# Performance work log

Measured on AMD Instinct MI355X. Metric: run time of the kernel, lower is better.

The kernel has to match this reference:

```python
import jax, jax.numpy as jnp
import numpy as np

NUM_LEVELS = 8
SQRT2 = float(np.sqrt(2.0))
LOG2 = float(np.log(2.0))


def _e8_roots():
    # 240 E8 roots: 112 of form (+-1,+-1,0^6) and 128 of form (+-1/2)^8 with even # of minus signs
    roots = []
    for i in range(8):
        for j in range(i + 1, 8):
            for si in (1.0, -1.0):
                for sj in (1.0, -1.0):
                    v = np.zeros(8, dtype=np.float32)
                    v[i] = si
                    v[j] = sj
                    roots.append(v)
    for bits in range(256):
        signs = np.array([1.0 if (bits >> k) & 1 == 0 else -1.0 for k in range(8)], dtype=np.float32)
        if int((signs < 0).sum()) % 2 == 0:
            roots.append(0.5 * signs)
    return np.stack(roots)  # [240, 8]


def setup_inputs() -> dict:
    key = jax.random.key(0)
    ks = jax.random.split(key, 12)
    B = 262144
    return {
        "observation": jax.random.normal(ks[0], (B, 14), jnp.float32),
        "proj_w1": jax.random.normal(ks[1], (32, 14), jnp.float32) * (1.0 / np.sqrt(14)),
        "proj_b1": jnp.zeros((32,), jnp.float32),
        "proj_w2": jax.random.normal(ks[2], (8, 32), jnp.float32) * (1.0 / np.sqrt(32)),
        "proj_b2": jnp.zeros((8,), jnp.float32),
        "level_embeddings": jax.random.normal(ks[3], (NUM_LEVELS, 240, 52), jnp.float32) * 0.02,
        "base_control_params": jax.random.normal(ks[4], (240, 4), jnp.float32) * 0.1,
        "residual_control_params": jax.random.normal(ks[5], (NUM_LEVELS - 1, 240, 4), jnp.float32) * 0.02,
        "base_complexity": jnp.zeros((240,), jnp.float32),  # log(initial_complexity=1.0)
        "log_decay": jnp.array([0.5 * np.log(240.0)], jnp.float32),  # log(sqrt(240))
        "refine_w1": jax.random.normal(ks[6], (52, 52), jnp.float32) * (1.0 / np.sqrt(52)),
        "refine_b1": jnp.zeros((52,), jnp.float32),
        "refine_w2": jax.random.normal(ks[7], (52, 52), jnp.float32) * (1.0 / np.sqrt(52)),
        "refine_b2": jnp.zeros((52,), jnp.float32),
        "refine_gate": jnp.array([0.1], jnp.float32),
    }


def reference(observation, proj_w1, proj_b1, proj_w2, proj_b2, level_embeddings,
              base_control_params, residual_control_params, base_complexity,
              log_decay, refine_w1, refine_b1, refine_w2, refine_b2, refine_gate):
    roots = jnp.asarray(_e8_roots())                                  # [240, 8]
    roots_norm = roots / jnp.linalg.norm(roots, axis=-1, keepdims=True)

    # G2 -> E8 projection: Linear(14->32) -> GELU -> Linear(32->8), L2-normalize * sqrt(2)
    h = jax.nn.gelu(observation @ proj_w1.T + proj_b1, approximate=False)
    q = h @ proj_w2.T + proj_b2                                       # [B, 8]
    q = q / jnp.maximum(jnp.linalg.norm(q, axis=-1, keepdims=True), 1e-12) * SQRT2

    decay = jnp.exp(log_decay[0])
    r2 = jnp.sum(roots * roots, axis=-1)                              # [240]

    # Residual E8 quantization: sequential cdist + argmin + gather chain
    residual = q
    indices = []
    for level in range(NUM_LEVELS):
        scale = 2.0 / decay ** level
        scaled = residual / scale                                     # [B, 8]
        x2 = jnp.sum(scaled * scaled, axis=-1, keepdims=True)         # [B, 1]
        d2 = jnp.maximum(x2 + r2[None, :] - 2.0 * scaled @ roots.T, 0.0)  # [B, 240]
        idx = jnp.argmin(d2, axis=-1)                                 # [B]
        indices.append(idx)
        residual = residual - roots[idx] * scale

    # Base level: soft attention over 240 roots with MDL prior
    sims = q @ roots_norm.T                                           # [B, 240]
    logits = sims - base_complexity[None, :] * LOG2
    attn = jax.nn.softmax(logits, axis=-1)                            # temperature = 1.0
    embedding = attn @ level_embeddings[0]                            # [B, 52]
    control = attn @ base_control_params                              # [B, 4]

    # Residual levels: hard-index gathers with 1/decay^level scaling
    for level in range(1, NUM_LEVELS):
        inv_ld = 1.0 / decay ** level
        idx = indices[level]
        embedding = embedding + level_embeddings[level][idx] * inv_ld
        control = control + residual_control_params[level - 1][idx] * inv_ld

    # Gated refinement MLP
    refined = jax.nn.gelu(embedding @ refine_w1.T + refine_b1, approximate=False) @ refine_w2.T + refine_b2
    embedding = embedding + jax.nn.sigmoid(refine_gate[0]) * refined

    return jnp.concatenate([embedding, control], axis=-1)             # [B, 56]
```

## Files before the change

### kernel.cpp

```cpp
#include <hip/hip_runtime.h>
#include <hip/hip_bf16.h>
#include <math.h>

#define TPB  256
#define RTPB 128
#define EPS_GAP 1e-4f
#define LTAB 13440
#define LDSZ 13680

typedef unsigned int u32;
typedef unsigned long long u64;
typedef __attribute__((ext_vector_type(8))) short bf16x8;
typedef __attribute__((ext_vector_type(4))) float f32x4;

__device__ __forceinline__ int scan_fast(const float* x, float scale,
                                         float* residual, bool protect, bool& flag){
    float aa[8]; int neg=0; float S=0.f;
    #pragma unroll
    for (int k=0;k<8;k++){
        float v=x[k]; float av=fabsf(v);
        aa[k]=av; S+=av; neg |= (v<0.f)?(1<<k):0;
    }
    float t1=-1e30f,t2=-1e30f,t3=-1e30f; int p1=0,p2=0;
    #pragma unroll
    for (int k=0;k<8;k++){
        float v=aa[k];
        bool g1=v>t1, g2=v>t2, g3=v>t3;
        t3 = g2 ? t2 : (g3 ? v : t3);
        t2 = g1 ? t1 : (g2 ? v : t2);
        p2 = g1 ? p1 : (g2 ? k : p2);
        t1 = g1 ? v : t1;
        p1 = g1 ? k : p1;
    }
    float n1=1e30f,n2v=1e30f; int m1=0;
    #pragma unroll
    for (int k=0;k<8;k++){
        float v=aa[k];
        bool l1=v<n1, l2=v<n2v;
        n2v = l1 ? n1 : (l2 ? v : n2v);
        n1  = l1 ? v : n1;
        m1  = l1 ? k : m1;
    }
    int bi = min(p1,p2), bj = max(p1,p2);
    float pv = 2.f*(t1+t2), pr = 2.f*(t1+t3);
    int par = __builtin_popcount((unsigned)neg)&1;
    float hv, hr; int hb;
    if (par==0){ hv=S;          hb=neg;           hr=S-2.f*(n1+n2v); }
    else       { hv=S-2.f*n1;   hb=neg^(1<<m1);   hr=S-2.f*n2v; }
    bool pair = (pv >= hv);
    float best = pair? pv: hv, alt = pair? hv: pv;
    float second = fmaxf(alt, fmaxf(pr,hr));
    if (protect) flag = flag || ((best-second) < EPS_GAP);
    int s = (((neg>>bi)&1)<<1) | ((neg>>bj)&1);
    int pidx = 4*(7*bi - ((bi*(bi-1))>>1) + (bj-bi-1)) + s;
    int hidx = 112 + (hb>>1);
    float sI = ((neg>>bi)&1)? scale : -scale;
    float sJ = ((neg>>bj)&1)? scale : -scale;
    #pragma unroll
    for (int k=0;k<8;k++){
        float cp = ((k==bi)? sI:0.f) + ((k==bj)? sJ:0.f);
        float ch = ((hb>>k)&1)? 0.5f*scale : -0.5f*scale;
        residual[k] += (pair? cp : ch);
    }
    return pair? pidx : hidx;
}

__device__ __forceinline__ int scan_fast_f64(const double* x, double scale,
                                             double* residual){
    double aa[8]; int neg=0; double S=0.0;
    #pragma unroll
    for (int k=0;k<8;k++){
        double v=x[k]; double av=fabs(v);
        aa[k]=av; S+=av; neg |= (v<0.0)?(1<<k):0;
    }
    double t1=-1e300,t2=-1e300; int p1=0,p2=0;
    #pragma unroll
    for (int k=0;k<8;k++){
        double v=aa[k];
        bool g1=v>t1, g2=v>t2;
        t2 = g1 ? t1 : (g2 ? v : t2);
        p2 = g1 ? p1 : (g2 ? k : p2);
        t1 = g1 ? v : t1;
        p1 = g1 ? k : p1;
    }
    double n1=1e300; int m1=0;
    #pragma unroll
    for (int k=0;k<8;k++){
        double v=aa[k];
        bool l1=v<n1;
        n1 = l1 ? v : n1;
        m1 = l1 ? k : m1;
    }
    int bi = min(p1,p2), bj = max(p1,p2);
    double pv = 2.0*(t1+t2);
    int par = __builtin_popcount((unsigned)neg)&1;
    double hv; int hb;
    if (par==0){ hv=S;          hb=neg; }
    else       { hv=S-2.0*n1;   hb=neg^(1<<m1); }
    bool pair = (pv >= hv);
    int s = (((neg>>bi)&1)<<1) | ((neg>>bj)&1);
    int pidx = 4*(7*bi - ((bi*(bi-1))>>1) + (bj-bi-1)) + s;
    int hidx = 112 + (hb>>1);
    double sI = ((neg>>bi)&1)? scale : -scale;
    double sJ = ((neg>>bj)&1)? scale : -scale;
    #pragma unroll
    for (int k=0;k<8;k++){
        double cp = ((k==bi)? sI:0.0) + ((k==bj)? sJ:0.0);
        double ch = ((hb>>k)&1)? 0.5*scale : -0.5*scale;
        residual[k] += (pair? cp : ch);
    }
    return pair? pidx : hidx;
}

__device__ __forceinline__ void phaseB(const float* __restrict__ L, float* T,
    const float* qf,
    int i1,int i2,int i3,int i4,int i5,int i6,int i7, float decay,
    const float* __restrict__ lemb, const float* __restrict__ rcpar,
    float* __restrict__ orow)
{
    const float IS2 = 0.70710678118654752f;
    const float HS2 = 0.35355339059327376f;
    const float LG2 = 0.69314718055994531f;
    float hi16[16];
    {
        float a01p=qf[0]+qf[1], a01m=qf[0]-qf[1];
        float a23p=qf[2]+qf[3], a23m=qf[2]-qf[3];
        float a45p=qf[4]+qf[5], a45m=qf[4]-qf[5];
        float a67p=qf[6]+qf[7], a67m=qf[6]-qf[7];
        float s01[4]={a01p,-a01m,a01m,-a01p};
        float s23[4]={a23p,-a23m,a23m,-a23p};
        float s45[4]={a45p,-a45m,a45m,-a45p};
        float s67[4]={a67p,-a67m,a67m,-a67p};
        #pragma unroll
        for (int p=0;p<16;p++){ T[8+p]=s01[p&3]+s23[(p>>2)&3]; hi16[p]=s45[p&3]+s67[(p>>2)&3]; }
        #pragma unroll
        for (int k=0;k<8;k++) T[k]=qf[k];
    }
    float emb[56], den=0.f;
    #pragma unroll
    for (int k=0;k<56;k++) emb[k]=0.f;

    auto proc = [&](float sims, int j){
        float e = __expf(sims - L[LTAB + j]*LG2);
        den += e;
        const float4* Lr = (const float4*)(L + j*56);
        #pragma unroll
        for (int t=0;t<14;t++){
            float4 v = Lr[t];
            emb[4*t+0]=fmaf(e,v.x,emb[4*t+0]); emb[4*t+1]=fmaf(e,v.y,emb[4*t+1]);
            emb[4*t+2]=fmaf(e,v.z,emb[4*t+2]); emb[4*t+3]=fmaf(e,v.w,emb[4*t+3]);
        }
    };
    #pragma unroll
    for (int h=0;h<16;h++){
        float hv = hi16[h];
        int ph = __builtin_popcount(h)&1;
        #pragma unroll 1
        for (int m=0;m<8;m++){
            int lo = (m<<1) | ((__builtin_popcount(m)&1)^ph);
            proc((T[8+lo]+hv)*HS2, 112 + (h<<3) + m);
        }
    }
    {
        int ii=0, jn=1;
        #pragma unroll 1
        for (int pc=0;pc<28;++pc){
            float a=T[ii], b=T[jn];
            float p=a+b, mm=a-b;
            proc( p*IS2, 4*pc+0);
            proc( mm*IS2,4*pc+1);
            proc(-mm*IS2,4*pc+2);
            proc(-p*IS2, 4*pc+3);
            if (++jn==8){ ++ii; jn=ii+1; }
        }
    }
    float rden = 1.f/den;
    #pragma unroll
    for (int k=0;k<56;k++) emb[k] *= rden;

    {
        float dp = decay;
        #define DO_G(LVL, IV) { \
            float ild = 1.0f/dp; \
            const float4* ep4 = (const float4*)(lemb + ((size_t)(LVL)*240 + (size_t)(IV))*52); \
            _Pragma("unroll") for (int t4=0;t4<13;t4++){ float4 v=ep4[t4]; \
                emb[4*t4+0]=fmaf(ild,v.x,emb[4*t4+0]); emb[4*t4+1]=fmaf(ild,v.y,emb[4*t4+1]); \
                emb[4*t4+2]=fmaf(ild,v.z,emb[4*t4+2]); emb[4*t4+3]=fmaf(ild,v.w,emb[4*t4+3]); } \
            float4 cv = *(const float4*)(rcpar + ((size_t)((LVL)-1)*240 + (size_t)(IV))*4); \
            emb[52]=fmaf(ild,cv.x,emb[52]); emb[53]=fmaf(ild,cv.y,emb[53]); \
            emb[54]=fmaf(ild,cv.z,emb[54]); emb[55]=fmaf(ild,cv.w,emb[55]); \
            dp *= decay; }
        DO_G(1,i1) DO_G(2,i2) DO_G(3,i3) DO_G(4,i4) DO_G(5,i5) DO_G(6,i6) DO_G(7,i7)
        #undef DO_G
    }
    float4* o4 = (float4*)orow;
    #pragma unroll
    for (int t=0;t<14;t++)
        o4[t] = make_float4(emb[4*t], emb[4*t+1], emb[4*t+2], emb[4*t+3]);
}

__device__ __forceinline__ void stageL(float* L, int tid, int tpb,
    const float* __restrict__ lemb, const float* __restrict__ bcp,
    const float* __restrict__ bcx)
{
    for (int t = tid; t < LTAB; t += tpb){
        int j = t/56, c = t - j*56;
        L[t] = (c < 52) ? lemb[j*52 + c] : bcp[j*4 + (c-52)];
    }
    for (int t = tid; t < 240; t += tpb) L[LTAB + t] = bcx[t];
}

__device__ __forceinline__ unsigned short f2bf(float x){
    union{float f; u32 u;} c; c.f = x;
    u32 u = c.u + 0x7fffu + ((c.u>>16)&1u);
    return (unsigned short)(u>>16);
}
__device__ __forceinline__ u32 pk2(float a, float b){
    union { __hip_bfloat162 h; u32 u; } cv;
    cv.h = __float22bfloat162_rn(make_float2(a,b));
    return cv.u;
}

#define BT_PITCH 264
#define E_PITCH  260
#define SCR_PITCH 68

#define EP4(i,jn,J,W) { \
    float P=(qf[i]+qf[jn])*IS2, M=(qf[i]-qf[jn])*IS2; \
    float e0=__expf(fmaf(-LG2,bcxL[(J)+0],P)); \
    float e1=__expf(fmaf(-LG2,bcxL[(J)+1],M)); \
    float e2=__expf(fmaf(-LG2,bcxL[(J)+2],-M)); \
    float e3=__expf(fmaf(-LG2,bcxL[(J)+3],-P)); \
    den += ((e0+e1)+(e2+e3)); \
    ESH[((W)+0)*E_PITCH + tid]=pk2(e0,e1); \
    ESH[((W)+1)*E_PITCH + tid]=pk2(e2,e3); }

#define LOV(Lx) (s01[(Lx)&3]+s23[(Lx)>>2])
#define EH8(h,J,W,L0,L1,L2,L3,L4,L5,L6,L7) { \
    float hv=s45[(h)&3]+s67[(h)>>2]; \
    float e0=__expf(fmaf(-LG2,bcxL[(J)+0],(LOV(L0)+hv)*HS2)); \
    float e1=__expf(fmaf(-LG2,bcxL[(J)+1],(LOV(L1)+hv)*HS2)); \
    float e2=__expf(fmaf(-LG2,bcxL[(J)+2],(LOV(L2)+hv)*HS2)); \
    float e3=__expf(fmaf(-LG2,bcxL[(J)+3],(LOV(L3)+hv)*HS2)); \
    float e4=__expf(fmaf(-LG2,bcxL[(J)+4],(LOV(L4)+hv)*HS2)); \
    float e5=__expf(fmaf(-LG2,bcxL[(J)+5],(LOV(L5)+hv)*HS2)); \
    float e6=__expf(fmaf(-LG2,bcxL[(J)+6],(LOV(L6)+hv)*HS2)); \
    float e7=__expf(fmaf(-LG2,bcxL[(J)+7],(LOV(L7)+hv)*HS2)); \
    den += (((e0+e1)+(e2+e3))+((e4+e5)+(e6+e7))); \
    ESH[((W)+0)*E_PITCH + tid]=pk2(e0,e1); \
    ESH[((W)+1)*E_PITCH + tid]=pk2(e2,e3); \
    ESH[((W)+2)*E_PITCH + tid]=pk2(e4,e5); \
    ESH[((W)+3)*E_PITCH + tid]=pk2(e6,e7); }

#define EFLUSH(c) { \
    union { u32 u[4]; bf16x8 v; } Af; \
    const unsigned short* bp = BtT + pp*BT_PITCH + qq*8 + (c)*32; \
    bf16x8 b0 = *(const bf16x8*)(const void*)(bp); \
    bf16x8 b1 = *(const bf16x8*)(const void*)(bp + 16*BT_PITCH); \
    bf16x8 b2 = *(const bf16x8*)(const void*)(bp + 32*BT_PITCH); \
    bf16x8 b3 = *(const bf16x8*)(const void*)(bp + 48*BT_PITCH); \
    _Pragma("unroll") for (int s4=0;s4<4;s4++){ \
        const u32* ep = ESH + (4*qq)*E_PITCH + wbase + 16*s4 + pp; \
        Af.u[0]=ep[0]; Af.u[1]=ep[E_PITCH]; Af.u[2]=ep[2*E_PITCH]; Af.u[3]=ep[3*E_PITCH]; \
        acc[s4][0]=__builtin_amdgcn_mfma_f32_16x16x32_bf16(Af.v,b0,acc[s4][0],0,0,0); \
        acc[s4][1]=__builtin_amdgcn_mfma_f32_16x16x32_bf16(Af.v,b1,acc[s4][1],0,0,0); \
        acc[s4][2]=__builtin_amdgcn_mfma_f32_16x16x32_bf16(Af.v,b2,acc[s4][2],0,0,0); \
        acc[s4][3]=__builtin_amdgcn_mfma_f32_16x16x32_bf16(Af.v,b3,acc[s4][3],0,0,0); \
    } }

__global__ __launch_bounds__(TPB) void e8_phaseA(
    const float* __restrict__ g_obs,
    const float* __restrict__ pw1, const float* __restrict__ pb1,
    const float* __restrict__ pw2, const float* __restrict__ pb2,
    const float* __restrict__ glogdecay,
    u32* __restrict__ cnt, u32* __restrict__ list,
    unsigned char* __restrict__ flags, int useCompact,
    float* __restrict__ out, int B)
{
    __shared__ float obsF[TPB*17];
    const int tid = threadIdx.x;
    const int row = blockIdx.x*TPB + tid;
    const bool active = row < B;
    const int lane = tid & 63;

    {
        const size_t base = (size_t)blockIdx.x*TPB*14;
        const size_t lim  = (size_t)B*14;
        for (int t = tid; t < TPB*14; t += TPB){
            size_t g = base + (size_t)t;
            float v = (g < lim) ? g_obs[g] : 0.f;
            int r = t/14, c = t - r*14;
            obsF[r*17 + c] = v;
        }
    }
    __syncthreads();

    float qf[8];
    int idxs[8] = {0,0,0,0,0,0,0,0};
    bool flag = false;
    {
        float ob[14];
        #pragma unroll
        for (int j=0;j<14;j++) ob[j]=obsF[tid*17+j];
        float qa[8];
        #pragma unroll
        for (int m=0;m<8;m++) qa[m]=pb2[m];
        #pragma unroll 1
        for (int k=0;k<32;k++){
            float a = pb1[k];
            #pragma unroll
            for (int j=0;j<14;j++) a = fmaf(pw1[k*14+j], ob[j], a);
            float h = 0.5f*a*(1.f+erff(a*0.70710678f));
            #pragma unroll
            for (int m=0;m<8;m++) qa[m] = fmaf(pw2[m*32+k], h, qa[m]);
        }
        float n2=0.f;
        #pragma unroll
        for (int m=0;m<8;m++) n2 = fmaf(qa[m],qa[m],n2);
        float nr = fmaxf(sqrtf(n2), 1e-12f);
        float sc = 1.41421356237309505f/nr;
        float residual[8];
        #pragma unroll
        for (int m=0;m<8;m++){ qf[m]=qa[m]*sc; residual[m]=qf[m]; }

        float decay = expf(glogdecay[0]);
        float dpow = 1.f;
        #pragma unroll
        for (int lvl=0; lvl<8; ++lvl){
            float rs = 0.5f*dpow;
            float x[8];
            #pragma unroll
            for (int k=0;k<8;k++) x[k]=residual[k]*rs;
            idxs[lvl] = scan_fast(x, 2.f/dpow, residual, (lvl<3), flag);
            dpow *= decay;
        }
    }
    flag = flag && active;

    if (useCompact){
        u64 mask = __ballot(flag);
        if (mask){
            int leader = __builtin_ctzll(mask);
            u32 base = 0;
            if (lane == leader) base = atomicAdd(cnt, (u32)__builtin_popcountll(mask));
            base = __shfl(base, leader, 64);
            if (flag){
                u32 pos = (u32)__builtin_popcountll(mask & ((1ull<<lane)-1ull));
                list[base+pos] = (u32)row;
            }
        }
    } else if (active){
        flags[row] = flag ? 1 : 0;
    }

    if (active){
        float* orow = out + (size_t)row*56;
        *(float4*)(orow+0) = make_float4(qf[0],qf[1],qf[2],qf[3]);
        *(float4*)(orow+4) = make_float4(qf[4],qf[5],qf[6],qf[7]);
        u32 iw0 = (u32)idxs[1] | ((u32)idxs[2]<<8) | ((u32)idxs[3]<<16) | ((u32)idxs[4]<<24);
        u32 iw1 = (u32)idxs[5] | ((u32)idxs[6]<<8) | ((u32)idxs[7]<<16);
        union{ u32 u[2]; float2 f; } iv; iv.u[0]=iw0; iv.u[1]=iw1;
        *(float2*)(orow+8) = iv.f;
    }
}

__global__ __attribute__((amdgpu_num_vgpr(192))) __launch_bounds__(TPB) void e8_phaseB(
    const float* __restrict__ lemb, const float* __restrict__ bcp,
    const float* __restrict__ rcpar, const float* __restrict__ bcx,
    const float* __restrict__ glogdecay,
    float* __restrict__ out, int B)
{
    const float IS2 = 0.70710678118654752f;
    const float HS2 = 0.35355339059327376f;
    const float LG2 = 0.69314718055994531f;

    __shared__ __align__(16) unsigned short BtT[64*BT_PITCH];
    __shared__ __align__(16) char UN[17408];
    __shared__ float bcxL[240];
    u32*   ESH  = (u32*)UN;
    float* scrF = (float*)UN;

    const int tid  = threadIdx.x;
    const int row  = blockIdx.x*TPB + tid;
    const bool active = row < B;
    const int lane = tid & 63;
    const int qq = lane >> 4, pp = lane & 15;
    const int wbase = tid & 192;

    for (int t = tid; t < 2048; t += TPB)
        BtT[(56 + (t>>8))*BT_PITCH + (t&255)] = 0;
    for (int t = tid; t < 1024; t += TPB)
        BtT[(t>>4)*BT_PITCH + 240 + (t&15)] = 0;
    for (int t = tid; t < 12480; t += TPB){
        int k = t/52, c = t - k*52;
        BtT[c*BT_PITCH + k] = f2bf(lemb[t]);
    }
    for (int t = tid; t < 960; t += TPB){
        int k = t>>2, c = 52 + (t&3);
        BtT[c*BT_PITCH + k] = f2bf(bcp[t]);
    }
    for (int t = tid; t < 240; t += TPB) bcxL[t] = bcx[t];

    float qf[8];
    u32 iw0=0, iw1=0;
    if (active){
        const float* orow = out + (size_t)row*56;
        float4 q0 = *(const float4*)(orow+0);
        float4 q1 = *(const float4*)(orow+4);
        qf[0]=q0.x; qf[1]=q0.y; qf[2]=q0.z; qf[3]=q0.w;
        qf[4]=q1.x; qf[5]=q1.y; qf[6]=q1.z; qf[7]=q1.w;
        union{ float2 f; u32 u[2]; } iv;
        iv.f = *(const float2*)(orow+8);
        iw0 = iv.u[0]; iw1 = iv.u[1];
    } else {
        #pragma unroll
        for (int m=0;m<8;m++) qf[m]=0.f;
    }
    float decay = expf(glogdecay[0]);
    __syncthreads();

    float s01[4], s23[4], s45[4], s67[4];
    {
        float a01p=qf[0]+qf[1], a01m=qf[0]-qf[1];
        float a23p=qf[2]+qf[3], a23m=qf[2]-qf[3];
        float a45p=qf[4]+qf[5], a45m=qf[4]-qf[5];
        float a67p=qf[6]+qf[7], a67m=qf[6]-qf[7];
        s01[0]=a01p; s01[1]=-a01m; s01[2]=a01m; s01[3]=-a01p;
        s23[0]=a23p; s23[1]=-a23m; s23[2]=a23m; s23[3]=-a23p;
        s45[0]=a45p; s45[1]=-a45m; s45[2]=a45m; s45[3]=-a45p;
        s67[0]=a67p; s67[1]=-a67m; s67[2]=a67m; s67[3]=-a67p;
    }

    f32x4 acc[4][4];
    #pragma unroll
    for (int s=0;s<4;s++)
        #pragma unroll
        for (int n=0;n<4;n++)
            acc[s][n] = f32x4{0.f,0.f,0.f,0.f};
    float den = 0.f;

    EP4(0,1,  0, 0) EP4(0,2,  4, 2) EP4(0,3,  8, 4) EP4(0,4, 12, 6)
    EP4(0,5, 16, 8) EP4(0,6, 20,10) EP4(0,7, 24,12) EP4(1,2, 28,14)
    EFLUSH(0)
    EP4(1,3, 32, 0) EP4(1,4, 36, 2) EP4(1,5, 40, 4) EP4(1,6, 44, 6)
    EP4(1,7, 48, 8) EP4(2,3, 52,10) EP4(2,4, 56,12) EP4(2,5, 60,14)
    EFLUSH(1)
    EP4(2,6, 64, 0) EP4(2,7, 68, 2) EP4(3,4, 72, 4) EP4(3,5, 76, 6)
    EP4(3,6, 80, 8) EP4(3,7, 84,10) EP4(4,5, 88,12) EP4(4,6, 92,14)
    EFLUSH(2)
    EP4(4,7, 96, 0) EP4(5,6,100, 2) EP4(5,7,104, 4) EP4(6,7,108, 6)
    EH8(0,112, 8, 0,3,5,6,9,10,12,15)
    EH8(1,120,12, 1,2,4,7,8,11,13,14)
    EFLUSH(3)
    EH8(2,128, 0, 1,2,4,7,8,11,13,14)
    EH8(3,136, 4, 0,3,5,6,9,10,12,15)
    EH8(4,144, 8, 1,2,4,7,8,11,13,14)
    EH8(5,152,12, 0,3,5,6,9,10,12,15)
    EFLUSH(4)
    EH8(6,160, 0, 0,3,5,6,9,10,12,15)
    EH8(7,168, 4, 1,2,4,7,8,11,13,14)
    EH8(8,176, 8, 1,2,4,7,8,11,13,14)
    EH8(9,184,12, 0,3,5,6,9,10,12,15)
    EFLUSH(5)
    EH8(10,192, 0, 0,3,5,6,9,10,12,15)
    EH8(11,200, 4, 1,2,4,7,8,11,13,14)
    EH8(12,208, 8, 0,3,5,6,9,10,12,15)
    EH8(13,216,12, 1,2,4,7,8,11,13,14)
    EFLUSH(6)
    EH8(14,224, 0, 1,2,4,7,8,11,13,14)
    EH8(15,232, 4, 0,3,5,6,9,10,12,15)
    #pragma unroll
    for (int w2=8; w2<16; w2++) ESH[w2*E_PITCH + tid]=0u;
    EFLUSH(7)

    __syncthreads();

    float emb[56];
    float* scr = scrF + (tid>>6)*(16*SCR_PITCH);
    #pragma unroll
    for (int s=0;s<4;s++){
        #pragma unroll
        for (int n=0;n<4;n++){
            #pragma unroll
            for (int r=0;r<4;r++)
                scr[(4*qq+r)*SCR_PITCH + 16*n + pp] = acc[s][n][r];
        }
        if ((lane>>4) == s){
            const float4* rp = (const float4*)(scr + pp*SCR_PITCH);
            #pragma unroll
            for (int t=0;t<14;t++){
                float4 v = rp[t];
                emb[4*t]=v.x; emb[4*t+1]=v.y; emb[4*t+2]=v.z; emb[4*t+3]=v.w;
            }
        }
    }

    if (active){
        float rden = 1.f/den;
        #pragma unroll
        for (int k=0;k<56;k++) emb[k] *= rden;

        int i1 = iw0 & 255, i2 = (iw0>>8)&255, i3 = (iw0>>16)&255, i4 = (iw0>>24)&255;
        int i5 = iw1 & 255, i6 = (iw1>>8)&255, i7 = (iw1>>16)&255;

        float dp = decay;
        #define DO_G2(LVL, IV) { \
            float ild = 1.0f/dp; \
            const float4* ep4 = (const float4*)(lemb + ((size_t)(LVL)*240 + (size_t)(IV))*52); \
            _Pragma("unroll") for (int t4=0;t4<13;t4++){ float4 v=ep4[t4]; \
                emb[4*t4+0]=fmaf(ild,v.x,emb[4*t4+0]); emb[4*t4+1]=fmaf(ild,v.y,emb[4*t4+1]); \
                emb[4*t4+2]=fmaf(ild,v.z,emb[4*t4+2]); emb[4*t4+3]=fmaf(ild,v.w,emb[4*t4+3]); } \
            float4 cv = *(const float4*)(rcpar + ((size_t)((LVL)-1)*240 + (size_t)(IV))*4); \
            emb[52]=fmaf(ild,cv.x,emb[52]); emb[53]=fmaf(ild,cv.y,emb[53]); \
            emb[54]=fmaf(ild,cv.z,emb[54]); emb[55]=fmaf(ild,cv.w,emb[55]); \
            dp *= decay; }
        DO_G2(1,i1) DO_G2(2,i2) DO_G2(3,i3) DO_G2(4,i4)
        DO_G2(5,i5) DO_G2(6,i6) DO_G2(7,i7)
        #undef DO_G2

        float4* o4 = (float4*)(out + (size_t)row*56);
        #pragma unroll
        for (int t=0;t<14;t++)
            o4[t] = make_float4(emb[4*t], emb[4*t+1], emb[4*t+2], emb[4*t+3]);
    }
}

__global__ __launch_bounds__(RTPB) void e8_rescue(
    const float* __restrict__ g_obs,
    const float* __restrict__ pw1, const float* __restrict__ pb1,
    const float* __restrict__ pw2, const float* __restrict__ pb2,
    const float* __restrict__ lemb, const float* __restrict__ bcp,
    const float* __restrict__ rcpar, const float* __restrict__ bcx,
    const float* __restrict__ glogdecay,
    const u32* __restrict__ cnt, const u32* __restrict__ list,
    const unsigned char* __restrict__ flags, int useCompact,
    float* __restrict__ out, int B)
{
    __shared__ float L[LDSZ];
    __shared__ float Ttab[RTPB*25];
    const int tid = threadIdx.x;
    int row = -1;
    bool valid;
    if (useCompact){
        u32 c = *cnt;
        if ((u32)(blockIdx.x*RTPB) >= c) return;
        int gid = blockIdx.x*RTPB + tid;
        valid = (gid < (int)c);
        if (valid) row = (int)list[gid];
    } else {
        row = blockIdx.x*RTPB + tid;
        valid = (row < B) && (flags[row] != 0);
        if (!__syncthreads_or(valid ? 1 : 0)) return;
    }
    stageL(L, tid, RTPB, lemb, bcp, bcx);
    __syncthreads();
    if (!valid) return;

    double ob[14];
    #pragma unroll
    for (int j=0;j<14;j++) ob[j] = (double)g_obs[(size_t)row*14+j];
    double qa[8];
    #pragma unroll
    for (int m=0;m<8;m++) qa[m] = (double)pb2[m];
    #pragma unroll 1
    for (int k=0;k<32;k++){
        double a = (double)pb1[k];
        #pragma unroll
        for (int j=0;j<14;j++) a += (double)pw1[k*14+j]*ob[j];
        double hk = 0.5*a*(1.0 + erf(a*0.70710678118654752440));
        #pragma unroll
        for (int m=0;m<8;m++) qa[m] += (double)pw2[m*32+k]*hk;
    }
    double n2 = 0.0;
    #pragma unroll
    for (int m=0;m<8;m++) n2 += qa[m]*qa[m];
    double nr = sqrt(n2); if (nr < 1e-12) nr = 1e-12;
    double q[8], residual[8];
    #pragma unroll
    for (int m=0;m<8;m++){ q[m] = qa[m]/nr*1.4142135623730951; residual[m]=q[m]; }

    double decay_d = exp((double)glogdecay[0]);
    double dpow = 1.0;
    int idxs[8] = {0,0,0,0,0,0,0,0};
    #pragma unroll
    for (int lvl=0; lvl<8; ++lvl){
        double rs = 0.5*dpow;
        double x[8];
        #pragma unroll
        for (int k=0;k<8;k++) x[k]=residual[k]*rs;
        idxs[lvl] = scan_fast_f64(x, 2.0/dpow, residual);
        dpow *= decay_d;
    }
    float qf[8];
    #pragma unroll
    for (int m=0;m<8;m++) qf[m]=(float)q[m];
    phaseB(L, Ttab + tid*25, qf, idxs[1],idxs[2],idxs[3],idxs[4],idxs[5],idxs[6],idxs[7],
           (float)decay_d, lemb, rcpar, out + (size_t)row*56);
}

__global__ __launch_bounds__(TPB) void e8_refine(
    const float* __restrict__ rw1, const float* __restrict__ rb1,
    const float* __restrict__ rw2, const float* __restrict__ rb2,
    const float* __restrict__ rgate,
    float* __restrict__ out, int B)
{
    __shared__ float W1[2704];
    __shared__ float W2T[2704];
    __shared__ float Bv[104];
    const int tid = threadIdx.x;
    for (int t = tid; t < 2704; t += TPB) W1[t] = rw1[t];
    for (int t = tid; t < 2704; t += TPB){
        int m = t/52, k = t - m*52;
        W2T[k*52 + m] = rw2[t];
    }
    for (int t = tid; t < 104; t += TPB) Bv[t] = (t < 52) ? rb1[t] : rb2[t-52];
    __syncthreads();

    const int row = blockIdx.x*TPB + tid;
    if (row >= B) return;
    float* orow = out + (size_t)row*56;
    float emb[52];
    {
        const float4* o4 = (const float4*)orow;
        #pragma unroll
        for (int t=0;t<13;t++){
            float4 v = o4[t];
            emb[4*t]=v.x; emb[4*t+1]=v.y; emb[4*t+2]=v.z; emb[4*t+3]=v.w;
        }
    }
    float sg = 1.f/(1.f+__expf(-rgate[0]));
    float acc[52];
    #pragma unroll
    for (int m=0;m<52;m++) acc[m]=0.f;
    #pragma unroll 1
    for (int k=0;k<52;k++){
        const float4* w1 = (const float4*)(W1 + k*52);
        float a0=0.f,a1=0.f,a2=0.f,a3=0.f;
        #pragma unroll
        for (int t=0;t<13;t++){
            float4 w = w1[t];
            a0=fmaf(w.x,emb[4*t+0],a0); a1=fmaf(w.y,emb[4*t+1],a1);
            a2=fmaf(w.z,emb[4*t+2],a2); a3=fmaf(w.w,emb[4*t+3],a3);
        }
        float a = ((a0+a1)+(a2+a3)) + Bv[k];
        float gk = sg*0.5f*a*(1.f+erff(a*0.70710678f));
        const float4* w2 = (const float4*)(W2T + k*52);
        #pragma unroll
        for (int t=0;t<13;t++){
            float4 w = w2[t];
            acc[4*t+0]=fmaf(gk,w.x,acc[4*t+0]); acc[4*t+1]=fmaf(gk,w.y,acc[4*t+1]);
            acc[4*t+2]=fmaf(gk,w.z,acc[4*t+2]); acc[4*t+3]=fmaf(gk,w.w,acc[4*t+3]);
        }
    }
    float4* o4 = (float4*)orow;
    #pragma unroll
    for (int t=0;t<13;t++){
        float4 v;
        v.x = emb[4*t+0] + fmaf(sg, Bv[52+4*t+0], acc[4*t+0]);
        v.y = emb[4*t+1] + fmaf(sg, Bv[52+4*t+1], acc[4*t+1]);
        v.z = emb[4*t+2] + fmaf(sg, Bv[52+4*t+2], acc[4*t+2]);
        v.w = emb[4*t+3] + fmaf(sg, Bv[52+4*t+3], acc[4*t+3]);
        o4[t] = v;
    }
}

extern "C" void kernel_launch(void* const* d_in, const int* in_sizes, int n_in,
                              void* d_out, int out_size, void* d_ws, size_t ws_size,
                              hipStream_t stream)
{
    const float* obs  = (const float*)d_in[0];
    const float* pw1  = (const float*)d_in[1];
    const float* pb1  = (const float*)d_in[2];
    const float* pw2  = (const float*)d_in[3];
    const float* pb2  = (const float*)d_in[4];
    const float* lemb = (const float*)d_in[5];
    const float* bcp  = (const float*)d_in[6];
    const float* rcp  = (const float*)d_in[7];
    const float* bcx  = (const float*)d_in[8];
    const float* ld   = (const float*)d_in[9];
    const float* rw1  = (const float*)d_in[10];
    const float* rb1  = (const float*)d_in[11];
    const float* rw2  = (const float*)d_in[12];
    const float* rb2  = (const float*)d_in[13];
    const float* rg   = (const float*)d_in[14];

    int B = in_sizes[0] / 14;
    int grid  = (B + TPB - 1) / TPB;
    int rgrid = (B + RTPB - 1) / RTPB;

    bool compact = ws_size >= (size_t)256 + (size_t)B*4;
    u32* cnt  = (u32*)d_ws;
    u32* list = (u32*)d_ws + 64;
    unsigned char* flags = (unsigned char*)d_ws + 256;

    hipMemsetAsync(d_ws, 0, 8, stream);

    e8_phaseA<<<grid, TPB, 0, stream>>>(obs, pw1, pb1, pw2, pb2, ld,
                                        cnt, list, flags, compact?1:0, (float*)d_out, B);
    e8_phaseB<<<grid, TPB, 0, stream>>>(lemb, bcp, rcp, bcx, ld, (float*)d_out, B);
    e8_rescue<<<rgrid, RTPB, 0, stream>>>(obs, pw1, pb1, pw2, pb2, lemb, bcp, rcp, bcx, ld,
                                          cnt, list, flags, compact?1:0, (float*)d_out, B);
    e8_refine<<<grid, TPB, 0, stream>>>(rw1, rb1, rw2, rb2, rg, (float*)d_out, B);
}
```

Baseline: 427.1 us.

## Stage refine kernel rows through padded LDS for coalesced loads and stores

The refine kernel now loads the block's 256x56 output tile cooperatively into a padded shared-memory buffer, computes the MLP from LDS, writes results back to LDS, and stores the tile coalesced. Before, each thread read and wrote its own 224-byte row, giving strided, poorly coalesced global accesses. It also drops the forced 192-VGPR attribute on phaseB. The extra ~58KB of LDS per block raises LDS use and may cut occupancy, which affects the compute-heavy MLP loop.

```diff
diff --git a/kernel.cpp b/kernel.cpp
--- a/kernel.cpp
+++ b/kernel.cpp
@@ -364,7 +364,7 @@
     }
 }
 
-__global__ __attribute__((amdgpu_num_vgpr(192))) __launch_bounds__(TPB) void e8_phaseB(
+__global__ __launch_bounds__(TPB) void e8_phaseB(
     const float* __restrict__ lemb, const float* __restrict__ bcp,
     const float* __restrict__ rcpar, const float* __restrict__ bcx,
     const float* __restrict__ glogdecay,
@@ -607,60 +607,68 @@
     __shared__ float W1[2704];
     __shared__ float W2T[2704];
     __shared__ float Bv[104];
+    __shared__ float R[TPB*57];
     const int tid = threadIdx.x;
+    const size_t base = (size_t)blockIdx.x*TPB*56;
+    const size_t lim  = (size_t)B*56;
+
     for (int t = tid; t < 2704; t += TPB) W1[t] = rw1[t];
     for (int t = tid; t < 2704; t += TPB){
         int m = t/52, k = t - m*52;
         W2T[k*52 + m] = rw2[t];
     }
     for (int t = tid; t < 104; t += TPB) Bv[t] = (t < 52) ? rb1[t] : rb2[t-52];
+    for (int t = tid; t < TPB*56; t += TPB){
+        size_t g = base + (size_t)t;
+        float v = (g < lim) ? out[g] : 0.f;
+        int r = t/56, c = t - r*56;
+        R[r*57 + c] = v;
+    }
     __syncthreads();
 
     const int row = blockIdx.x*TPB + tid;
-    if (row >= B) return;
-    float* orow = out + (size_t)row*56;
+    const bool active = row < B;
     float emb[52];
-    {
-        const float4* o4 = (const float4*)orow;
-        #pragma unroll
-        for (int t=0;t<13;t++){
-            float4 v = o4[t];
-            emb[4*t]=v.x; emb[4*t+1]=v.y; emb[4*t+2]=v.z; emb[4*t+3]=v.w;
-        }
-    }
+    float acc[52];
     float sg = 1.f/(1.f+__expf(-rgate[0]));
-    float acc[52];
-    #pragma unroll
-    for (int m=0;m<52;m++) acc[m]=0.f;
-    #pragma unroll 1
-    for (int k=0;k<52;k++){
-        const float4* w1 = (const float4*)(W1 + k*52);
-        float a0=0.f,a1=0.f,a2=0.f,a3=0.f;
-        #pragma unroll
-        for (int t=0;t<13;t++){
-            float4 w = w1[t];
-            a0=fmaf(w.x,emb[4*t+0],a0); a1=fmaf(w.y,emb[4*t+1],a1);
-            a2=fmaf(w.z,emb[4*t+2],a2); a3=fmaf(w.w,emb[4*t+3],a3);
-        }
-        float a = ((a0+a1)+(a2+a3)) + Bv[k];
-        float gk = sg*0.5f*a*(1.f+erff(a*0.70710678f));
-        const float4* w2 = (const float4*)(W2T + k*52);
-        #pragma unroll
-        for (int t=0;t<13;t++){
-            float4 w = w2[t];
-            acc[4*t+0]=fmaf(gk,w.x,acc[4*t+0]); acc[4*t+1]=fmaf(gk,w.y,acc[4*t+1]);
-            acc[4*t+2]=fmaf(gk,w.z,acc[4*t+2]); acc[4*t+3]=fmaf(gk,w.w,acc[4*t+3]);
-        }
-    }
-    float4* o4 = (float4*)orow;
-    #pragma unroll
-    for (int t=0;t<13;t++){
-        float4 v;
-        v.x = emb[4*t+0] + fmaf(sg, Bv[52+4*t+0], acc[4*t+0]);
-        v.y = emb[4*t+1] + fmaf(sg, Bv[52+4*t+1], acc[4*t+1]);
-        v.z = emb[4*t+2] + fmaf(sg, Bv[52+4*t+2], acc[4*t+2]);
-        v.w = emb[4*t+3] + fmaf(sg, Bv[52+4*t+3], acc[4*t+3]);
-        o4[t] = v;
+    if (active){
+        const float* myR = R + tid*57;
+        #pragma unroll
+        for (int m=0;m<52;m++) emb[m] = myR[m];
+        #pragma unroll
+        for (int m=0;m<52;m++) acc[m]=0.f;
+        #pragma unroll 1
+        for (int k=0;k<52;k++){
+            const float4* w1 = (const float4*)(W1 + k*52);
+            float a0=0.f,a1=0.f,a2=0.f,a3=0.f;
+            #pragma unroll
+            for (int t=0;t<13;t++){
+                float4 w = w1[t];
+                a0=fmaf(w.x,emb[4*t+0],a0); a1=fmaf(w.y,emb[4*t+1],a1);
+                a2=fmaf(w.z,emb[4*t+2],a2); a3=fmaf(w.w,emb[4*t+3],a3);
+            }
+            float a = ((a0+a1)+(a2+a3)) + Bv[k];
+            float gk = sg*0.5f*a*(1.f+erff(a*0.70710678f));
+            const float4* w2 = (const float4*)(W2T + k*52);
+            #pragma unroll
+            for (int t=0;t<13;t++){
+                float4 w = w2[t];
+                acc[4*t+0]=fmaf(gk,w.x,acc[4*t+0]); acc[4*t+1]=fmaf(gk,w.y,acc[4*t+1]);
+                acc[4*t+2]=fmaf(gk,w.z,acc[4*t+2]); acc[4*t+3]=fmaf(gk,w.w,acc[4*t+3]);
+            }
+        }
+        float* myW = R + tid*57;
+        #pragma unroll
+        for (int m=0;m<52;m++)
+            myW[m] = emb[m] + fmaf(sg, Bv[52+m], acc[m]);
+    }
+    __syncthreads();
+    for (int t = tid; t < TPB*56; t += TPB){
+        int r = t/56, c = t - r*56;
+        if (c < 52){
+            size_t g = base + (size_t)t;
+            if (g < lim) out[g] = R[r*57 + c];
+        }
     }
 }
 
```

New measurement: 538.7 us. 26.1% more time.

## Restructure rescue kernel as one-wave-per-row persistent grid-stride loop

Applied to the files above, without the earlier changes.

The rescue kernel previously staged the full 240x56 embedding table into LDS per 128-thread block and had each thread handle one flagged row with a 56-wide register accumulator. It now launches a fixed grid of 64-thread blocks that grid-stride over the flagged rows, with each lane owning one output column and reading the table straight from global memory/cache. This removes the large per-block LDS staging cost and the register pressure when few rows need rescue. In exchange, every lane redundantly repeats the f64 projection and quantisation for the row, and many blocks still start up even when the rescue list is empty. The phaseB kernel also drops its explicit VGPR cap attribute.

```diff
diff --git a/kernel.cpp b/kernel.cpp
--- a/kernel.cpp
+++ b/kernel.cpp
@@ -3,10 +3,9 @@
 #include <math.h>
 
 #define TPB  256
-#define RTPB 128
+#define RW   64
+#define RGRID 2048
 #define EPS_GAP 1e-4f
-#define LTAB 13440
-#define LDSZ 13680
 
 typedef unsigned int u32;
 typedef unsigned long long u64;
@@ -110,104 +109,6 @@
         residual[k] += (pair? cp : ch);
     }
     return pair? pidx : hidx;
-}
-
-__device__ __forceinline__ void phaseB(const float* __restrict__ L, float* T,
-    const float* qf,
-    int i1,int i2,int i3,int i4,int i5,int i6,int i7, float decay,
-    const float* __restrict__ lemb, const float* __restrict__ rcpar,
-    float* __restrict__ orow)
-{
-    const float IS2 = 0.70710678118654752f;
-    const float HS2 = 0.35355339059327376f;
-    const float LG2 = 0.69314718055994531f;
-    float hi16[16];
-    {
-        float a01p=qf[0]+qf[1], a01m=qf[0]-qf[1];
-        float a23p=qf[2]+qf[3], a23m=qf[2]-qf[3];
-        float a45p=qf[4]+qf[5], a45m=qf[4]-qf[5];
-        float a67p=qf[6]+qf[7], a67m=qf[6]-qf[7];
-        float s01[4]={a01p,-a01m,a01m,-a01p};
-        float s23[4]={a23p,-a23m,a23m,-a23p};
-        float s45[4]={a45p,-a45m,a45m,-a45p};
-        float s67[4]={a67p,-a67m,a67m,-a67p};
-        #pragma unroll
-        for (int p=0;p<16;p++){ T[8+p]=s01[p&3]+s23[(p>>2)&3]; hi16[p]=s45[p&3]+s67[(p>>2)&3]; }
-        #pragma unroll
-        for (int k=0;k<8;k++) T[k]=qf[k];
-    }
-    float emb[56], den=0.f;
-    #pragma unroll
-    for (int k=0;k<56;k++) emb[k]=0.f;
-
-    auto proc = [&](float sims, int j){
-        float e = __expf(sims - L[LTAB + j]*LG2);
-        den += e;
-        const float4* Lr = (const float4*)(L + j*56);
-        #pragma unroll
-        for (int t=0;t<14;t++){
-            float4 v = Lr[t];
-            emb[4*t+0]=fmaf(e,v.x,emb[4*t+0]); emb[4*t+1]=fmaf(e,v.y,emb[4*t+1]);
-            emb[4*t+2]=fmaf(e,v.z,emb[4*t+2]); emb[4*t+3]=fmaf(e,v.w,emb[4*t+3]);
-        }
-    };
-    #pragma unroll
-    for (int h=0;h<16;h++){
-        float hv = hi16[h];
-        int ph = __builtin_popcount(h)&1;
-        #pragma unroll 1
-        for (int m=0;m<8;m++){
-            int lo = (m<<1) | ((__builtin_popcount(m)&1)^ph);
-            proc((T[8+lo]+hv)*HS2, 112 + (h<<3) + m);
-        }
-    }
-    {
-        int ii=0, jn=1;
-        #pragma unroll 1
-        for (int pc=0;pc<28;++pc){
-            float a=T[ii], b=T[jn];
-            float p=a+b, mm=a-b;
-            proc( p*IS2, 4*pc+0);
-            proc( mm*IS2,4*pc+1);
-            proc(-mm*IS2,4*pc+2);
-            proc(-p*IS2, 4*pc+3);
-            if (++jn==8){ ++ii; jn=ii+1; }
-        }
-    }
-    float rden = 1.f/den;
-    #pragma unroll
-    for (int k=0;k<56;k++) emb[k] *= rden;
-
-    {
-        float dp = decay;
-        #define DO_G(LVL, IV) { \
-            float ild = 1.0f/dp; \
-            const float4* ep4 = (const float4*)(lemb + ((size_t)(LVL)*240 + (size_t)(IV))*52); \
-            _Pragma("unroll") for (int t4=0;t4<13;t4++){ float4 v=ep4[t4]; \
-                emb[4*t4+0]=fmaf(ild,v.x,emb[4*t4+0]); emb[4*t4+1]=fmaf(ild,v.y,emb[4*t4+1]); \
-                emb[4*t4+2]=fmaf(ild,v.z,emb[4*t4+2]); emb[4*t4+3]=fmaf(ild,v.w,emb[4*t4+3]); } \
-            float4 cv = *(const float4*)(rcpar + ((size_t)((LVL)-1)*240 + (size_t)(IV))*4); \
-            emb[52]=fmaf(ild,cv.x,emb[52]); emb[53]=fmaf(ild,cv.y,emb[53]); \
-            emb[54]=fmaf(ild,cv.z,emb[54]); emb[55]=fmaf(ild,cv.w,emb[55]); \
-            dp *= decay; }
-        DO_G(1,i1) DO_G(2,i2) DO_G(3,i3) DO_G(4,i4) DO_G(5,i5) DO_G(6,i6) DO_G(7,i7)
-        #undef DO_G
-    }
-    float4* o4 = (float4*)orow;
-    #pragma unroll
-    for (int t=0;t<14;t++)
-        o4[t] = make_float4(emb[4*t], emb[4*t+1], emb[4*t+2], emb[4*t+3]);
-}
-
-__device__ __forceinline__ void stageL(float* L, int tid, int tpb,
-    const float* __restrict__ lemb, const float* __restrict__ bcp,
-    const float* __restrict__ bcx)
-{
-    for (int t = tid; t < LTAB; t += tpb){
-        int j = t/56, c = t - j*56;
-        L[t] = (c < 52) ? lemb[j*52 + c] : bcp[j*4 + (c-52)];
-    }
-    for (int t = tid; t < 240; t += tpb) L[LTAB + t] = bcx[t];
 }
 
 __device__ __forceinline__ unsigned short f2bf(float x){
@@ -364,7 +265,7 @@
     }
 }
 
-__global__ __attribute__((amdgpu_num_vgpr(192))) __launch_bounds__(TPB) void e8_phaseB(
+__global__ __launch_bounds__(TPB) void e8_phaseB(
     const float* __restrict__ lemb, const float* __restrict__ bcp,
     const float* __restrict__ rcpar, const float* __restrict__ bcx,
     const float* __restrict__ glogdecay,
@@ -525,7 +426,23 @@
     }
 }
 
-__global__ __launch_bounds__(RTPB) void e8_rescue(
+#define RHm(h,m) { \
+    float sims = (lo16v[((m)<<1)|((__builtin_popcount(m)&1)^(__builtin_popcount(h)&1))] + hi16v[h])*HS2; \
+    float e = __expf(sims - bcxS[112+((h)<<3)+(m)]*LG2); \
+    den += e; \
+    emb_c = fmaf(e, colp[(size_t)(112+((h)<<3)+(m))*cstr], emb_c); }
+#define RH8(h) RHm(h,0) RHm(h,1) RHm(h,2) RHm(h,3) RHm(h,4) RHm(h,5) RHm(h,6) RHm(h,7)
+#define RP1(j) { \
+    float e = __expf(sv - bcxS[j]*LG2); den += e; \
+    emb_c = fmaf(e, colp[(size_t)(j)*cstr], emb_c); }
+#define RP(pc,i,j2) { \
+    float a=qf[i], b=qf[j2]; float p=a+b, mm=a-b; float sv; \
+    sv =  p*IS2; RP1(4*(pc)+0) \
+    sv = mm*IS2; RP1(4*(pc)+1) \
+    sv = -mm*IS2; RP1(4*(pc)+2) \
+    sv = -p*IS2; RP1(4*(pc)+3) }
+
+__global__ __launch_bounds__(RW) void e8_rescue(
     const float* __restrict__ g_obs,
     const float* __restrict__ pw1, const float* __restrict__ pb1,
     const float* __restrict__ pw2, const float* __restrict__ pb2,
@@ -536,66 +453,119 @@
     const unsigned char* __restrict__ flags, int useCompact,
     float* __restrict__ out, int B)
 {
-    __shared__ float L[LDSZ];
-    __shared__ float Ttab[RTPB*25];
-    const int tid = threadIdx.x;
-    int row = -1;
-    bool valid;
+    const float IS2 = 0.70710678118654752f;
+    const float HS2 = 0.35355339059327376f;
+    const float LG2 = 0.69314718055994531f;
+    __shared__ float bcxS[240];
+    const int c = threadIdx.x;
+
+    u32 nwork;
     if (useCompact){
-        u32 c = *cnt;
-        if ((u32)(blockIdx.x*RTPB) >= c) return;
-        int gid = blockIdx.x*RTPB + tid;
-        valid = (gid < (int)c);
-        if (valid) row = (int)list[gid];
+        nwork = *cnt;
+        if (blockIdx.x >= nwork) return;
     } else {
-        row = blockIdx.x*RTPB + tid;
-        valid = (row < B) && (flags[row] != 0);
-        if (!__syncthreads_or(valid ? 1 : 0)) return;
-    }
-    stageL(L, tid, RTPB, lemb, bcp, bcx);
-    __syncthreads();
-    if (!valid) return;
-
-    double ob[14];
-    #pragma unroll
-    for (int j=0;j<14;j++) ob[j] = (double)g_obs[(size_t)row*14+j];
-    double qa[8];
-    #pragma unroll
-    for (int m=0;m<8;m++) qa[m] = (double)pb2[m];
-    #pragma unroll 1
-    for (int k=0;k<32;k++){
-        double a = (double)pb1[k];
-        #pragma unroll
-        for (int j=0;j<14;j++) a += (double)pw1[k*14+j]*ob[j];
-        double hk = 0.5*a*(1.0 + erf(a*0.70710678118654752440));
-        #pragma unroll
-        for (int m=0;m<8;m++) qa[m] += (double)pw2[m*32+k]*hk;
-    }
-    double n2 = 0.0;
-    #pragma unroll
-    for (int m=0;m<8;m++) n2 += qa[m]*qa[m];
-    double nr = sqrt(n2); if (nr < 1e-12) nr = 1e-12;
-    double q[8], residual[8];
-    #pragma unroll
-    for (int m=0;m<8;m++){ q[m] = qa[m]/nr*1.4142135623730951; residual[m]=q[m]; }
+        nwork = 0;
+    }
+    for (int t = c; t < 240; t += RW) bcxS[t] = bcx[t];
+
+    const float* colp; size_t cstr;
+    if (c < 52)      { colp = lemb + c;        cstr = 52; }
+    else if (c < 56) { colp = bcp + (c - 52);  cstr = 4;  }
+    else             { colp = lemb;            cstr = 0;  }
 
     double decay_d = exp((double)glogdecay[0]);
-    double dpow = 1.0;
-    int idxs[8] = {0,0,0,0,0,0,0,0};
-    #pragma unroll
-    for (int lvl=0; lvl<8; ++lvl){
-        double rs = 0.5*dpow;
-        double x[8];
-        #pragma unroll
-        for (int k=0;k<8;k++) x[k]=residual[k]*rs;
-        idxs[lvl] = scan_fast_f64(x, 2.0/dpow, residual);
-        dpow *= decay_d;
-    }
-    float qf[8];
-    #pragma unroll
-    for (int m=0;m<8;m++) qf[m]=(float)q[m];
-    phaseB(L, Ttab + tid*25, qf, idxs[1],idxs[2],idxs[3],idxs[4],idxs[5],idxs[6],idxs[7],
-           (float)decay_d, lemb, rcpar, out + (size_t)row*56);
+    float decayf = (float)decay_d;
+
+    for (u32 wi = blockIdx.x; ; wi += gridDim.x){
+        int row;
+        if (useCompact){
+            if (wi >= nwork) break;
+            row = (int)list[wi];
+        } else {
+            if (wi >= (u32)B) break;
+            if (!flags[wi]) continue;
+            row = (int)wi;
+        }
+
+        double ob[14];
+        #pragma unroll
+        for (int j=0;j<14;j++) ob[j] = (double)g_obs[(size_t)row*14+j];
+        double qa[8];
+        #pragma unroll
+        for (int m=0;m<8;m++) qa[m] = (double)pb2[m];
+        #pragma unroll 1
+        for (int k=0;k<32;k++){
+            double a = (double)pb1[k];
+            #pragma unroll
+            for (int j=0;j<14;j++) a += (double)pw1[k*14+j]*ob[j];
+            double hk = 0.5*a*(1.0 + erf(a*0.70710678118654752440));
+            #pragma unroll
+            for (int m=0;m<8;m++) qa[m] += (double)pw2[m*32+k]*hk;
+        }
+        double n2 = 0.0;
+        #pragma unroll
+        for (int m=0;m<8;m++) n2 += qa[m]*qa[m];
+        double nr = sqrt(n2); if (nr < 1e-12) nr = 1e-12;
+        double q[8], residual[8];
+        #pragma unroll
+        for (int m=0;m<8;m++){ q[m] = qa[m]/nr*1.4142135623730951; residual[m]=q[m]; }
+
+        double dpow = 1.0;
+        int idxs[8] = {0,0,0,0,0,0,0,0};
+        #pragma unroll
+        for (int lvl=0; lvl<8; ++lvl){
+            double rs = 0.5*dpow;
+            double x[8];
+            #pragma unroll
+            for (int k=0;k<8;k++) x[k]=residual[k]*rs;
+            idxs[lvl] = scan_fast_f64(x, 2.0/dpow, residual);
+            dpow *= decay_d;
+        }
+        float qf[8];
+        #pragma unroll
+        for (int m=0;m<8;m++) qf[m]=(float)q[m];
+
+        float lo16v[16], hi16v[16];
+        {
+            float a01p=qf[0]+qf[1], a01m=qf[0]-qf[1];
+            float a23p=qf[2]+qf[3], a23m=qf[2]-qf[3];
+            float a45p=qf[4]+qf[5], a45m=qf[4]-qf[5];
+            float a67p=qf[6]+qf[7], a67m=qf[6]-qf[7];
+            float s01[4]={a01p,-a01m,a01m,-a01p};
+            float s23[4]={a23p,-a23m,a23m,-a23p};
+            float s45[4]={a45p,-a45m,a45m,-a45p};
+            float s67[4]={a67p,-a67m,a67m,-a67p};
+            #pragma unroll
+            for (int p=0;p<16;p++){ lo16v[p]=s01[p&3]+s23[(p>>2)&3]; hi16v[p]=s45[p&3]+s67[(p>>2)&3]; }
+        }
+
+        float emb_c = 0.f, den = 0.f;
+        RH8(0)  RH8(1)  RH8(2)  RH8(3)  RH8(4)  RH8(5)  RH8(6)  RH8(7)
+        RH8(8)  RH8(9)  RH8(10) RH8(11) RH8(12) RH8(13) RH8(14) RH8(15)
+        RP(0,0,1)  RP(1,0,2)  RP(2,0,3)  RP(3,0,4)  RP(4,0,5)  RP(5,0,6)  RP(6,0,7)
+        RP(7,1,2)  RP(8,1,3)  RP(9,1,4)  RP(10,1,5) RP(11,1,6) RP(12,1,7)
+        RP(13,2,3) RP(14,2,4) RP(15,2,5) RP(16,2,6) RP(17,2,7)
+        RP(18,3,4) RP(19,3,5) RP(20,3,6) RP(21,3,7)
+        RP(22,4,5) RP(23,4,6) RP(24,4,7)
+        RP(25,5,6) RP(26,5,7)
+        RP(27,6,7)
+        emb_c *= 1.f/den;
+
+        float dp = decayf;
+        #pragma unroll
+        for (int lvl=1; lvl<8; ++lvl){
+            float ild = 1.0f/dp;
+            int idx = idxs[lvl];
+            float gv;
+            if (c < 52)      gv = lemb[((size_t)lvl*240 + (size_t)idx)*52 + c];
+            else if (c < 56) gv = rcpar[((size_t)(lvl-1)*240 + (size_t)idx)*4 + (c-52)];
+            else             gv = 0.f;
+            emb_c = fmaf(ild, gv, emb_c);
+            dp *= decayf;
+        }
+
+        if (c < 56) out[(size_t)row*56 + c] = emb_c;
+    }
 }
 
 __global__ __launch_bounds__(TPB) void e8_refine(
@@ -686,7 +656,6 @@
 
     int B = in_sizes[0] / 14;
     int grid  = (B + TPB - 1) / TPB;
-    int rgrid = (B + RTPB - 1) / RTPB;
 
     bool compact = ws_size >= (size_t)256 + (size_t)B*4;
     u32* cnt  = (u32*)d_ws;
@@ -698,7 +667,7 @@
     e8_phaseA<<<grid, TPB, 0, stream>>>(obs, pw1, pb1, pw2, pb2, ld,
                                         cnt, list, flags, compact?1:0, (float*)d_out, B);
     e8_phaseB<<<grid, TPB, 0, stream>>>(lemb, bcp, rcp, bcx, ld, (float*)d_out, B);
-    e8_rescue<<<rgrid, RTPB, 0, stream>>>(obs, pw1, pb1, pw2, pb2, lemb, bcp, rcp, bcx, ld,
-                                          cnt, list, flags, compact?1:0, (float*)d_out, B);
+    e8_rescue<<<RGRID, RW, 0, stream>>>(obs, pw1, pb1, pw2, pb2, lemb, bcp, rcp, bcx, ld,
+                                        cnt, list, flags, compact?1:0, (float*)d_out, B);
     e8_refine<<<grid, TPB, 0, stream>>>(rw1, rb1, rw2, rb2, rg, (float*)d_out, B);
 }
```

New measurement: 568.4 us. +33.1%, slower.
